# Performance work log

Hardware: AMD Instinct MI355X
Metric: run time of the kernel (lower is better)

## Reference

```python
import jax, jax.numpy as jnp
import numpy as np

N = 1024
H = 1024
B, T = 64, 256


def setup_inputs() -> dict:
    key = jax.random.key(0)
    ks = jax.random.split(key, 12)
    inp = {
        "h_time": jax.random.normal(ks[0], (B, T, H), dtype=jnp.float32),
        "A_pearson": jax.random.uniform(ks[1], (N, N), dtype=jnp.float32),
        "E_dyn": jax.random.normal(ks[2], (N, H), dtype=jnp.float32) * 0.1,
        "alpha_raw": jnp.float32(0.5),
        "tau_raw": jnp.float32(1.0),
        # gate_gen: Linear(H, H//2) -> GELU -> Linear(H//2, N) -> Sigmoid
        "gate_W1": jax.random.normal(ks[3], (H, H // 2), dtype=jnp.float32) * (1.0 / np.sqrt(H)),
        "gate_b1": jnp.zeros((H // 2,), dtype=jnp.float32),
        "gate_W2": jax.random.normal(ks[4], (H // 2, N), dtype=jnp.float32) * (1.0 / np.sqrt(H // 2)),
        "gate_b2": jnp.zeros((N,), dtype=jnp.float32),
        "h2n_W": jax.random.normal(ks[5], (H, N), dtype=jnp.float32) * (1.0 / np.sqrt(H)),
        "h2n_b": jnp.zeros((N,), dtype=jnp.float32),
        "n2h_W": jax.random.normal(ks[6], (N, H), dtype=jnp.float32) * (1.0 / np.sqrt(N)),
        "n2h_b": jnp.zeros((H,), dtype=jnp.float32),
        "ln_w": jnp.ones((H,), dtype=jnp.float32),
        "ln_b": jnp.zeros((H,), dtype=jnp.float32),
    }
    return inp


def _layernorm(x, w, b, eps=1e-5):
    mu = x.mean(-1, keepdims=True)
    var = ((x - mu) ** 2).mean(-1, keepdims=True)
    return (x - mu) * jax.lax.rsqrt(var + eps) * w + b


def reference(h_time, A_pearson, E_dyn, alpha_raw, tau_raw,
              gate_W1, gate_b1, gate_W2, gate_b2,
              h2n_W, h2n_b, n2h_W, n2h_b, ln_w, ln_b):
    tau = jax.nn.softplus(tau_raw) + 1e-6
    alpha = jax.nn.sigmoid(alpha_raw)

    h_mean = h_time.mean(axis=(0, 1))                      # [H]
    E = E_dyn + h_mean[None, :]
    E_cur = E / jnp.maximum(jnp.linalg.norm(E, axis=-1, keepdims=True), 1e-12)  # F.normalize

    A_dyn = jax.nn.relu(E_cur @ E_cur.T)                   # [N,N]
    A_dyn = A_dyn / (A_dyn.sum(axis=-1, keepdims=True) + 1e-6)
    A_dyn = 0.5 * (A_dyn + A_dyn.T)
    A_base = alpha * A_pearson + (1.0 - alpha) * A_dyn

    h_gate = h_time.mean(axis=1)                           # [B,H]
    hid = jax.nn.gelu(h_gate @ gate_W1 + gate_b1, approximate=False)
    gamma = jax.nn.sigmoid(hid @ gate_W2 + gate_b2)        # [B,N]

    # Python loop over batch == row-scaling by mean gate
    A_mix = A_base * gamma.mean(axis=0)[:, None]           # [N,N]

    z_nodes = h_time @ h2n_W + h2n_b                       # [B,T,N]
    z_gcn = jnp.einsum('btn,mn->btm', z_nodes, A_mix)      # z_nodes @ A_mix.T
    msg_h = z_gcn @ n2h_W + n2h_b                          # [B,T,H]

    logits = (A_base @ E_cur) / tau                        # [N,H]
    node_attn = jax.nn.softmax(logits, axis=0)
    global_w = jnp.tanh(node_attn.mean(axis=0))            # [H]

    y = h_time * (1.0 + global_w) + msg_h
    return _layernorm(y, ln_w, ln_b)
```

## Files before the change

kernel.cpp:

```cpp
#include <hip/hip_runtime.h>
#include <math.h>

#define H 1024
#define Nn 1024
#define Bb 64
#define Tt 256
#define BT (Bb * Tt)

typedef unsigned short ushort_t;
typedef __attribute__((ext_vector_type(8))) short bf16x8;
typedef __attribute__((ext_vector_type(4))) float f32x4;


__device__ __forceinline__ ushort_t f2bf(float x) {
    union { float f; unsigned u; } v; v.f = x;
    unsigned r = v.u + 0x7FFFu + ((v.u >> 16) & 1u);
    return (ushort_t)(r >> 16);
}
__device__ __forceinline__ float bf2f(ushort_t h) {
    union { unsigned u; float f; } v; v.u = ((unsigned)h) << 16; return v.f;
}

__device__ __forceinline__ float block_reduce_sum_256(float v) {
    __shared__ float sbuf[4];
    __syncthreads();
    #pragma unroll
    for (int off = 32; off > 0; off >>= 1) v += __shfl_down(v, off, 64);
    int lane = threadIdx.x & 63, w = threadIdx.x >> 6;
    if (lane == 0) sbuf[w] = v;
    __syncthreads();
    if (threadIdx.x == 0) sbuf[0] = sbuf[0] + sbuf[1] + sbuf[2] + sbuf[3];
    __syncthreads();
    return sbuf[0];
}

__global__ void k_stage1(const float* __restrict__ h_time, float* __restrict__ hg_part,
                         ushort_t* __restrict__ ht_bf16, const float* __restrict__ n2h_b,
                         float* __restrict__ rowsumS, float* __restrict__ bias_h,
                         const float* __restrict__ n2h_W, const float* __restrict__ h2n_W,
                         const float* __restrict__ W1, const float* __restrict__ W2,
                         ushort_t* __restrict__ n2hWT_h, ushort_t* __restrict__ n2hWT_l,
                         ushort_t* __restrict__ h2nW_h, ushort_t* __restrict__ h2nW_l,
                         float* __restrict__ W1T, float* __restrict__ W2T) {
    __shared__ float tile[32][33];
    int id = blockIdx.x;
    if (id < 2048) {
        int b = id >> 5, r = id & 31;
        int z = r >> 2, cb = r & 3;
        int col = cb * 256 + threadIdx.x;
        if (b == 0 && z == 0) {
            rowsumS[col] = 0.f;
            bias_h[col] = n2h_b[col];
        }
        float s = 0.f;
        #pragma unroll 4
        for (int t = z * 32; t < z * 32 + 32; ++t) {
            size_t o = ((size_t)b * Tt + t) * H + col;
            float v = h_time[o];
            s += v;
            ht_bf16[o] = f2bf(v);
        }
        hg_part[(size_t)(b * 8 + z) * H + col] = s;
        return;
    }
    int tx = threadIdx.x & 31, ty = threadIdx.x >> 5;
    if (id < 3072) {
        int t = id - 2048;
        int i0 = (t >> 5) * 32, j0 = (t & 31) * 32;
        #pragma unroll
        for (int q = 0; q < 4; ++q)
            tile[ty + 8 * q][tx] = n2h_W[(size_t)(i0 + ty + 8 * q) * H + j0 + tx];
        __syncthreads();
        #pragma unroll
        for (int q = 0; q < 4; ++q) {
            float v = tile[tx][ty + 8 * q];
            size_t o = (size_t)(j0 + ty + 8 * q) * Nn + i0 + tx;
            ushort_t hh = f2bf(v);
            n2hWT_h[o] = hh;
            n2hWT_l[o] = f2bf(v - bf2f(hh));
        }
    } else if (id < 4096) {
        size_t idx = (size_t)(id - 3072) * 1024 + threadIdx.x * 4;
        float4 v = *(const float4*)&h2n_W[idx];
        float c[4] = {v.x, v.y, v.z, v.w};
        union { ushort_t u[4]; uint2 w; } ph, pl;
        #pragma unroll
        for (int q = 0; q < 4; ++q) {
            ph.u[q] = f2bf(c[q]);
            pl.u[q] = f2bf(c[q] - bf2f(ph.u[q]));
        }
        *(uint2*)&h2nW_h[idx] = ph.w;
        *(uint2*)&h2nW_l[idx] = pl.w;
    } else if (id < 4608) {
        int t = id - 4096;
        int i0 = (t >> 4) * 32, j0 = (t & 15) * 32;
        #pragma unroll
        for (int q = 0; q < 4; ++q)
            tile[ty + 8 * q][tx] = W1[(size_t)(i0 + ty + 8 * q) * 512 + j0 + tx];
        __syncthreads();
        #pragma unroll
        for (int q = 0; q < 4; ++q)
            W1T[(size_t)(j0 + ty + 8 * q) * 1024 + i0 + tx] = tile[tx][ty + 8 * q];
    } else {
        int t = id - 4608;
        int i0 = (t >> 5) * 32, j0 = (t & 31) * 32;
        #pragma unroll
        for (int q = 0; q < 4; ++q)
            tile[ty + 8 * q][tx] = W2[(size_t)(i0 + ty + 8 * q) * 1024 + j0 + tx];
        __syncthreads();
        #pragma unroll
        for (int q = 0; q < 4; ++q)
            W2T[(size_t)(j0 + ty + 8 * q) * 512 + i0 + tx] = tile[tx][ty + 8 * q];
    }
}

__global__ void k_stage2(const float* __restrict__ hg_part, float* __restrict__ h_gate,
                         float* __restrict__ h_mean) {
    int id = blockIdx.x;
    if (id < 256) {
        int b = id >> 2, cb = id & 3;
        int col = cb * 256 + threadIdx.x;
        float s = 0.f;
        #pragma unroll
        for (int z = 0; z < 8; ++z) s += hg_part[(size_t)(b * 8 + z) * H + col];
        h_gate[b * H + col] = s * (1.0f / Tt);
    } else {
        int h = (id - 256) * 256 + threadIdx.x;
        float s = 0.f;
        for (int r = 0; r < 512; ++r) s += hg_part[(size_t)r * H + h];
        h_mean[h] = s * (1.0f / (Bb * Tt));
    }
}

__global__ __launch_bounds__(256) void k_stage3(
    const float* __restrict__ E_dyn, const float* __restrict__ h_mean,
    ushort_t* __restrict__ E_b,
    const float* __restrict__ h_gate, const float* __restrict__ W1T,
    const float* __restrict__ b1, float* __restrict__ hid) {
    if (blockIdx.x < 1024) {
        int n = blockIdx.x;
        float e[4]; float ss = 0.f;
        #pragma unroll
        for (int q = 0; q < 4; ++q) {
            int h = threadIdx.x + 256 * q;
            e[q] = E_dyn[(size_t)n * H + h] + h_mean[h];
            ss += e[q] * e[q];
        }
        float tot = block_reduce_sum_256(ss);
        float scale = 1.0f / fmaxf(sqrtf(tot), 1e-12f);
        #pragma unroll
        for (int q = 0; q < 4; ++q) {
            int h = threadIdx.x + 256 * q;
            E_b[(size_t)n * H + h] = f2bf(e[q] * scale);
        }
        return;
    }
    int gid = (blockIdx.x - 1024) * 4 + (threadIdx.x >> 6);
    int lane = threadIdx.x & 63;
    int b = gid >> 9, j = gid & 511;
    const float* xr = h_gate + b * H;
    const float* wr = W1T + (size_t)j * H;
    float s = 0.f;
    #pragma unroll
    for (int it = 0; it < 4; ++it) {
        int k = it * 256 + lane * 4;
        float4 x4 = *(const float4*)&xr[k];
        float4 w4 = *(const float4*)&wr[k];
        s += x4.x * w4.x + x4.y * w4.y + x4.z * w4.z + x4.w * w4.w;
    }
    #pragma unroll
    for (int off = 32; off > 0; off >>= 1) s += __shfl_down(s, off, 64);
    if (lane == 0) {
        float a = s + b1[j];
        hid[b * 512 + j] = 0.5f * a * (1.0f + erff(a * 0.70710678118654752f));
    }
}

template <int PASSES, int EPI>
__device__ __forceinline__ void gemm64_body(
    int bx, int by,
    const ushort_t* __restrict__ Ah, const ushort_t* __restrict__ Al,
    const ushort_t* __restrict__ Bh, const ushort_t* __restrict__ Bl,
    ushort_t* __restrict__ O1, ushort_t* __restrict__ O2,
    float* __restrict__ fout, const float* __restrict__ fvec,
    int M, int N, int K) {
    constexpr int NST = (PASSES == 3) ? 4 : 2;
    constexpr int BUFSZ = NST * 64 * 64;
    __shared__ ushort_t sStage[2 * BUFSZ];
    const int tid = threadIdx.x, wave = tid >> 6, lane = tid & 63;
    const int quad = lane >> 4, l16 = lane & 15;
    const int m0 = by * 64, n0 = bx * 64;
    const int wm = (wave >> 1) * 32, wn = (wave & 1) * 32;
    const int sw = (l16 & 7) << 3;

    f32x4 acc[2][2];
    #pragma unroll
    for (int i = 0; i < 2; ++i)
        #pragma unroll
        for (int j = 0; j < 2; ++j)
            acc[i][j] = (f32x4){0.f, 0.f, 0.f, 0.f};

    auto stage = [&](int buf, int k0) {
        ushort_t* sAh = sStage + buf * BUFSZ;
        ushort_t* sBh = sAh + 64 * 64;
        ushort_t* sAl = sAh + 2 * 64 * 64;
        ushort_t* sBl = sAh + 3 * 64 * 64;
        #pragma unroll
        for (int inst = 0; inst < 2; ++inst) {
            const int cbase = (wave * 2 + inst) * 64;
            const int c = cbase + lane;
            const int row = c >> 3;
            const int q = (c & 7) ^ (row & 7);
            const size_t offA = (size_t)(m0 + row) * K + k0 + q * 8;
            const size_t offB = (size_t)(n0 + row) * K + k0 + q * 8;
            __builtin_amdgcn_global_load_lds(
                (const __attribute__((address_space(1))) unsigned int*)(Ah + offA),
                (__attribute__((address_space(3))) unsigned int*)&sAh[cbase * 8], 16, 0, 0);
            __builtin_amdgcn_global_load_lds(
                (const __attribute__((address_space(1))) unsigned int*)(Bh + offB),
                (__attribute__((address_space(3))) unsigned int*)&sBh[cbase * 8], 16, 0, 0);
            if constexpr (PASSES == 3) {
                __builtin_amdgcn_global_load_lds(
                    (const __attribute__((address_space(1))) unsigned int*)(Al + offA),
                    (__attribute__((address_space(3))) unsigned int*)&sAl[cbase * 8], 16, 0, 0);
                __builtin_amdgcn_global_load_lds(
                    (const __attribute__((address_space(1))) unsigned int*)(Bl + offB),
                    (__attribute__((address_space(3))) unsigned int*)&sBl[cbase * 8], 16, 0, 0);
            }
        }
    };

    auto compute = [&](int buf) {
        const ushort_t* sAh = sStage + buf * BUFSZ;
        const ushort_t* sBh = sAh + 64 * 64;
        const ushort_t* sAl = sAh + 2 * 64 * 64;
        const ushort_t* sBl = sAh + 3 * 64 * 64;
        #pragma unroll
        for (int half = 0; half < 2; ++half) {
            bf16x8 fah[2], fbh[2];
            bf16x8 fal[PASSES == 3 ? 2 : 1], fbl[PASSES == 3 ? 2 : 1];
            #pragma unroll
            for (int i = 0; i < 2; ++i) {
                const int ko = ((half * 4 + quad) << 3) ^ sw;
                fah[i] = *(const bf16x8*)&sAh[(wm + i * 16 + l16) * 64 + ko];
                fbh[i] = *(const bf16x8*)&sBh[(wn + i * 16 + l16) * 64 + ko];
                if constexpr (PASSES == 3) {
                    fal[i] = *(const bf16x8*)&sAl[(wm + i * 16 + l16) * 64 + ko];
                    fbl[i] = *(const bf16x8*)&sBl[(wn + i * 16 + l16) * 64 + ko];
                }
            }
            #pragma unroll
            for (int i = 0; i < 2; ++i)
                #pragma unroll
                for (int j = 0; j < 2; ++j) {
                    acc[i][j] = __builtin_amdgcn_mfma_f32_16x16x32_bf16(fah[i], fbh[j], acc[i][j], 0, 0, 0);
                    if constexpr (PASSES == 3) {
                        acc[i][j] = __builtin_amdgcn_mfma_f32_16x16x32_bf16(fah[i], fbl[j], acc[i][j], 0, 0, 0);
                        acc[i][j] = __builtin_amdgcn_mfma_f32_16x16x32_bf16(fal[i], fbh[j], acc[i][j], 0, 0, 0);
                    }
                }
        }
    };

    stage(0, 0);
    __syncthreads();
    int cur = 0;
    for (int k0 = 64; k0 < K; k0 += 64) {
        stage(cur ^ 1, k0);
        compute(cur);
        __syncthreads();
        cur ^= 1;
    }
    compute(cur);

    float fv[2];
    if constexpr (EPI == 2) {
        #pragma unroll
        for (int j = 0; j < 2; ++j) fv[j] = fvec[n0 + wn + j * 16 + l16];
    }
    #pragma unroll
    for (int i = 0; i < 2; ++i)
        #pragma unroll
        for (int r = 0; r < 4; ++r) {
            const int m = m0 + wm + i * 16 + quad * 4 + r;
            float rowacc = 0.f;
            #pragma unroll
            for (int j = 0; j < 2; ++j) {
                const size_t o = (size_t)m * N + n0 + wn + j * 16 + l16;
                float v = acc[i][j][r];
                if constexpr (EPI == 1) {
                    v = fmaxf(v, 0.f);
                    O1[o] = f2bf(v);
                    rowacc += v;
                } else if constexpr (EPI == 2) {
                    ushort_t hh = f2bf(v);
                    O1[o] = hh;
                    O2[o] = f2bf(v - bf2f(hh));
                    rowacc += v * fv[j];
                } else {
                    O1[o] = f2bf(v);
                }
            }
            if constexpr (EPI == 1 || EPI == 2) {
                rowacc += __shfl_xor(rowacc, 1);
                rowacc += __shfl_xor(rowacc, 2);
                rowacc += __shfl_xor(rowacc, 4);
                rowacc += __shfl_xor(rowacc, 8);
                if (l16 == 0) atomicAdd(&fout[m], rowacc);
            }
        }
}

__global__ __launch_bounds__(256) void k_stage4(
    const float* __restrict__ hid, const float* __restrict__ W2T,
    const float* __restrict__ b2, float* __restrict__ gmean,
    const ushort_t* __restrict__ E_b, ushort_t* __restrict__ Sb,
    float* __restrict__ rowsumS) {
    if (blockIdx.x < 256) {
        int n = blockIdx.x * 4 + (threadIdx.x >> 6);
        int lane = threadIdx.x & 63;
        const float* wr = W2T + (size_t)n * 512;
        float4 w0 = *(const float4*)&wr[lane * 4];
        float4 w1 = *(const float4*)&wr[256 + lane * 4];
        float bb = b2[n];
        float acc = 0.f;
        for (int b = 0; b < Bb; ++b) {
            const float* xr = hid + b * 512;
            float4 x0 = *(const float4*)&xr[lane * 4];
            float4 x1 = *(const float4*)&xr[256 + lane * 4];
            float s = x0.x * w0.x + x0.y * w0.y + x0.z * w0.z + x0.w * w0.w
                    + x1.x * w1.x + x1.y * w1.y + x1.z * w1.z + x1.w * w1.w;
            #pragma unroll
            for (int off = 32; off > 0; off >>= 1) s += __shfl_down(s, off, 64);
            if (lane == 0) acc += 1.0f / (1.0f + expf(-(s + bb)));
        }
        if (lane == 0) gmean[n] = acc * (1.0f / Bb);
        return;
    }
    int t = blockIdx.x - 256;
    gemm64_body<1, 1>(t & 15, t >> 4, E_b, nullptr, E_b, nullptr,
                      Sb, nullptr, rowsumS, nullptr, Nn, Nn, H);
}

__global__ void k_amixT(const ushort_t* __restrict__ Sb, const float* __restrict__ A_p,
                        const float* __restrict__ rowsumS, const float* __restrict__ gmean,
                        const float* __restrict__ alpha_raw,
                        ushort_t* __restrict__ Th, ushort_t* __restrict__ Tl) {
    __shared__ float tile[32][33];
    int i0 = blockIdx.y * 32, j0 = blockIdx.x * 32;
    int tx = threadIdx.x & 31, ty = threadIdx.x >> 5;
    float alpha = 1.0f / (1.0f + expf(-alpha_raw[0]));
    #pragma unroll
    for (int q = 0; q < 4; ++q) {
        int i = i0 + ty + 8 * q, j = j0 + tx;
        size_t idx = (size_t)i * Nn + j;
        float s = bf2f(Sb[idx]);
        float ad = 0.5f * s * (1.0f / (rowsumS[i] + 1e-6f) + 1.0f / (rowsumS[j] + 1e-6f));
        tile[ty + 8 * q][tx] = gmean[i] * fmaf(alpha, A_p[idx], (1.0f - alpha) * ad);
    }
    __syncthreads();
    #pragma unroll
    for (int q = 0; q < 4; ++q) {
        float v = tile[tx][ty + 8 * q];
        size_t o = (size_t)(j0 + ty + 8 * q) * Nn + i0 + tx;
        ushort_t hh = f2bf(v);
        Th[o] = hh;
        Tl[o] = f2bf(v - bf2f(hh));
    }
}

__global__ __launch_bounds__(256) void k_c1t(
    const ushort_t* __restrict__ Ah, const ushort_t* __restrict__ Al,
    const ushort_t* __restrict__ Bh, const ushort_t* __restrict__ Bl,
    ushort_t* __restrict__ O1, ushort_t* __restrict__ O2,
    float* __restrict__ fout, const float* __restrict__ fvec) {
    gemm64_body<3, 2>(blockIdx.x & 15, blockIdx.x >> 4, Ah, Al, Bh, Bl, O1, O2, fout, fvec,
                      Nn, Nn, Nn);
}
__global__ __launch_bounds__(256) void k_c2t(
    const ushort_t* __restrict__ Ah, const ushort_t* __restrict__ Al,
    const ushort_t* __restrict__ Bh, const ushort_t* __restrict__ Bl,
    ushort_t* __restrict__ O1) {
    gemm64_body<3, 3>(blockIdx.x & 15, blockIdx.x >> 4, Ah, Al, Bh, Bl, O1, nullptr,
                      nullptr, nullptr, Nn, Nn, Nn);
}

__global__ __launch_bounds__(256) void gemm_big(
    const ushort_t* __restrict__ A, const ushort_t* __restrict__ Bt,
    float* __restrict__ fout, const float* __restrict__ fvec,
    int M, int N, int K) {
    constexpr int BUFSZ = 2 * 128 * 64;
    __shared__ ushort_t sStage[2 * BUFSZ];

    const int tid = threadIdx.x;
    const int wave = tid >> 6, lane = tid & 63;
    const int quad = lane >> 4, l16 = lane & 15;
    int bx = blockIdx.x, g = bx & 7, s = bx >> 3;
    const int m0 = (g * 16 + (s >> 3)) * 128;
    const int n0 = (s & 7) * 128;
    const int wm = (wave >> 1) * 64, wn = (wave & 1) * 64;
    const int sw = (l16 & 7) << 3;

    f32x4 acc[4][4];
    #pragma unroll
    for (int i = 0; i < 4; ++i)
        #pragma unroll
        for (int j = 0; j < 4; ++j)
            acc[i][j] = (f32x4){0.f, 0.f, 0.f, 0.f};

    auto stage = [&](int buf, int k0) {
        ushort_t* sAh = sStage + buf * BUFSZ;
        ushort_t* sBh = sAh + 128 * 64;
        #pragma unroll
        for (int inst = 0; inst < 4; ++inst) {
            const int cbase = (wave * 4 + inst) * 64;
            const int c = cbase + lane;
            const int row = c >> 3;
            const int q = (c & 7) ^ (row & 7);
            const size_t offA = (size_t)(m0 + row) * K + k0 + q * 8;
            const size_t offB = (size_t)(n0 + row) * K + k0 + q * 8;
            __builtin_amdgcn_global_load_lds(
                (const __attribute__((address_space(1))) unsigned int*)(A + offA),
                (__attribute__((address_space(3))) unsigned int*)&sAh[cbase * 8], 16, 0, 0);
            __builtin_amdgcn_global_load_lds(
                (const __attribute__((address_space(1))) unsigned int*)(Bt + offB),
                (__attribute__((address_space(3))) unsigned int*)&sBh[cbase * 8], 16, 0, 0);
        }
    };

    auto compute = [&](int buf) {
        const ushort_t* sAh = sStage + buf * BUFSZ;
        const ushort_t* sBh = sAh + 128 * 64;
        #pragma unroll
        for (int half = 0; half < 2; ++half) {
            bf16x8 fah[4], fbh[4];
            #pragma unroll
            for (int i = 0; i < 4; ++i) {
                const int ko = ((half * 4 + quad) << 3) ^ sw;
                fah[i] = *(const bf16x8*)&sAh[(wm + i * 16 + l16) * 64 + ko];
                fbh[i] = *(const bf16x8*)&sBh[(wn + i * 16 + l16) * 64 + ko];
            }
            #pragma unroll
            for (int i = 0; i < 4; ++i)
                #pragma unroll
                for (int j = 0; j < 4; ++j)
                    acc[i][j] = __builtin_amdgcn_mfma_f32_16x16x32_bf16(fah[i], fbh[j], acc[i][j], 0, 0, 0);
        }
    };

    stage(0, 0);
    __syncthreads();
    int cur = 0;
    for (int k0 = 64; k0 < K; k0 += 64) {
        stage(cur ^ 1, k0);
        compute(cur);
        __syncthreads();
        cur ^= 1;
    }
    compute(cur);
    __syncthreads();

    float* EsW = (float*)sStage + wave * 4096;
    const float SC = 1.0009765622f;

    #pragma unroll
    for (int i = 0; i < 4; ++i)
        #pragma unroll
        for (int j = 0; j < 4; ++j)
            #pragma unroll
            for (int r = 0; r < 4; ++r)
                EsW[i * 1024 + (quad * 4 + r) * 64 + j * 16 + l16] = acc[i][j][r];
    __syncthreads();
    #pragma unroll
    for (int i = 0; i < 4; ++i) {
        #pragma unroll
        for (int it = 0; it < 4; ++it) {
            const int idx = it * 64 + lane;
            const int row = idx >> 4, f4 = idx & 15;
            const int m = m0 + wm + i * 16 + row;
            const int coln = n0 + wn + f4 * 4;
            float4 v = *(const float4*)&EsW[i * 1024 + row * 64 + f4 * 4];
            float4 b4 = *(const float4*)&fvec[coln];
            ushort4 h4 = *(const ushort4*)&A[(size_t)m * N + coln];
            float4 y;
            y.x = v.x + b4.x + SC * bf2f(h4.x);
            y.y = v.y + b4.y + SC * bf2f(h4.y);
            y.z = v.z + b4.z + SC * bf2f(h4.z);
            y.w = v.w + b4.w + SC * bf2f(h4.w);
            *(float4*)&fout[(size_t)m * N + coln] = y;
        }
    }
}

__global__ __launch_bounds__(256) void k_final_ln(const float* __restrict__ ln_w,
                                                  const float* __restrict__ ln_b,
                                                  float* __restrict__ out) {
    int wave = threadIdx.x >> 6, lane = threadIdx.x & 63;
    size_t row = (size_t)blockIdx.x * 4 + wave;
    float4 v[4];
    float s = 0.f;
    #pragma unroll
    for (int q = 0; q < 4; ++q) {
        v[q] = *(const float4*)&out[row * H + q * 256 + lane * 4];
        s += v[q].x + v[q].y + v[q].z + v[q].w;
    }
    #pragma unroll
    for (int off = 1; off < 64; off <<= 1) s += __shfl_xor(s, off, 64);
    float mu = s * (1.0f / H);
    float ss = 0.f;
    #pragma unroll
    for (int q = 0; q < 4; ++q) {
        v[q].x -= mu; v[q].y -= mu; v[q].z -= mu; v[q].w -= mu;
        ss += v[q].x * v[q].x + v[q].y * v[q].y + v[q].z * v[q].z + v[q].w * v[q].w;
    }
    #pragma unroll
    for (int off = 1; off < 64; off <<= 1) ss += __shfl_xor(ss, off, 64);
    float rstd = rsqrtf(ss * (1.0f / H) + 1e-5f);
    #pragma unroll
    for (int q = 0; q < 4; ++q) {
        int k = q * 256 + lane * 4;
        float4 w4 = *(const float4*)&ln_w[k];
        float4 b4 = *(const float4*)&ln_b[k];
        float4 o;
        o.x = fmaf(v[q].x * rstd, w4.x, b4.x);
        o.y = fmaf(v[q].y * rstd, w4.y, b4.y);
        o.z = fmaf(v[q].z * rstd, w4.z, b4.z);
        o.w = fmaf(v[q].w * rstd, w4.w, b4.w);
        *(float4*)&out[row * H + k] = o;
    }
}


extern "C" void kernel_launch(void* const* d_in, const int* in_sizes, int n_in,
                              void* d_out, int out_size, void* d_ws, size_t ws_size,
                              hipStream_t stream) {
    const float* h_time    = (const float*)d_in[0];
    const float* A_p       = (const float*)d_in[1];
    const float* E_dyn     = (const float*)d_in[2];
    const float* alpha_raw = (const float*)d_in[3];
    const float* gW1   = (const float*)d_in[5];
    const float* gb1   = (const float*)d_in[6];
    const float* gW2   = (const float*)d_in[7];
    const float* gb2   = (const float*)d_in[8];
    const float* h2n_W = (const float*)d_in[9];
    const float* h2n_b = (const float*)d_in[10];
    const float* n2h_W = (const float*)d_in[11];
    const float* n2h_b = (const float*)d_in[12];
    const float* ln_w  = (const float*)d_in[13];
    const float* ln_b  = (const float*)d_in[14];
    float* out = (float*)d_out;

    float* ws = (float*)d_ws;
    float* h_gate  = ws;  ws += Bb * H;
    float* h_mean  = ws;  ws += H;
    float* rowsumS = ws;  ws += Nn;
    float* bias_h  = ws;  ws += H;
    float* hid     = ws;  ws += Bb * 512;
    float* gmean   = ws;  ws += Nn;
    float* W1T     = ws;  ws += 512 * H;
    float* W2T     = ws;  ws += H * 512;
    float* hg_part = ws;  ws += 512 * H;
    ws += 256;
    ushort_t* E_b     = (ushort_t*)ws;  ws += (Nn * H) / 2;
    ushort_t* Sb      = (ushort_t*)ws;  ws += (Nn * Nn) / 2;
    ushort_t* AmixT_h = (ushort_t*)ws;  ws += (Nn * Nn) / 2;
    ushort_t* AmixT_l = (ushort_t*)ws;  ws += (Nn * Nn) / 2;
    ushort_t* n2hWT_h = (ushort_t*)ws;  ws += (Nn * H) / 2;
    ushort_t* n2hWT_l = (ushort_t*)ws;  ws += (Nn * H) / 2;
    ushort_t* h2nW_h  = (ushort_t*)ws;  ws += (H * Nn) / 2;
    ushort_t* h2nW_l  = (ushort_t*)ws;  ws += (H * Nn) / 2;
    ushort_t* C1Th    = (ushort_t*)ws;  ws += (H * Nn) / 2;
    ushort_t* C1Tl    = (ushort_t*)ws;  ws += (H * Nn) / 2;
    ushort_t* C2t     = (ushort_t*)ws;  ws += (H * H) / 2;
    ushort_t* ht      = (ushort_t*)ws;  ws += ((size_t)BT * H) / 2;

    k_stage1<<<5120, 256, 0, stream>>>(h_time, hg_part, ht, n2h_b, rowsumS, bias_h,
                                       n2h_W, h2n_W, gW1, gW2,
                                       n2hWT_h, n2hWT_l, h2nW_h, h2nW_l, W1T, W2T);
    k_stage2<<<260, 256, 0, stream>>>(hg_part, h_gate, h_mean);
    k_stage3<<<9216, 256, 0, stream>>>(E_dyn, h_mean, E_b, h_gate, W1T, gb1, hid);
    k_stage4<<<512, 256, 0, stream>>>(hid, W2T, gb2, gmean, E_b, Sb, rowsumS);
    k_amixT<<<dim3(32, 32), 256, 0, stream>>>(Sb, A_p, rowsumS, gmean, alpha_raw, AmixT_h, AmixT_l);
    k_c1t<<<256, 256, 0, stream>>>(n2hWT_h, n2hWT_l, AmixT_h, AmixT_l, C1Th, C1Tl, bias_h, h2n_b);
    k_c2t<<<256, 256, 0, stream>>>(C1Th, C1Tl, h2nW_h, h2nW_l, C2t);
    gemm_big<<<1024, 256, 0, stream>>>(ht, C2t, out, bias_h, BT, H, H);
    k_final_ln<<<4096, 256, 0, stream>>>(ln_w, ln_b, out);
}
```

Baseline: 316.6 us.

## Enlarge big GEMM tiles to 256x256 with 8 waves and barrier-synchronized MFMA phases

The main BTxHxH bf16 GEMM moves from 128x128 tiles with 4 waves to 256x256 tiles with 8 waves, so each wave computes a 128x64 sub-tile. The k-loop is restructured with explicit s_barrier, waitcnt and setprio around MFMA bursts so waves interleave LDS reads and matrix math. The epilogue is split into two passes to fit the larger tile in LDS. The aim is to raise arithmetic intensity and cut global/L2 traffic per FLOP. The cost is only 256 blocks (about one wave of work on the GPU), higher register pressure, and a dropped grouped-tile swizzle for L2 locality.

```diff
diff --git a/kernel.cpp b/kernel.cpp
--- a/kernel.cpp
+++ b/kernel.cpp
@@ -385,110 +385,126 @@
                       nullptr, nullptr, Nn, Nn, Nn);
 }
 
-__global__ __launch_bounds__(256) void gemm_big(
+__global__ __launch_bounds__(512, 2) void gemm_big(
     const ushort_t* __restrict__ A, const ushort_t* __restrict__ Bt,
     float* __restrict__ fout, const float* __restrict__ fvec,
     int M, int N, int K) {
-    constexpr int BUFSZ = 2 * 128 * 64;
+    constexpr int BUFSZ = 2 * 256 * 64;
     __shared__ ushort_t sStage[2 * BUFSZ];
 
     const int tid = threadIdx.x;
     const int wave = tid >> 6, lane = tid & 63;
     const int quad = lane >> 4, l16 = lane & 15;
-    int bx = blockIdx.x, g = bx & 7, s = bx >> 3;
-    const int m0 = (g * 16 + (s >> 3)) * 128;
-    const int n0 = (s & 7) * 128;
-    const int wm = (wave >> 1) * 64, wn = (wave & 1) * 64;
-    const int sw = (l16 & 7) << 3;
-
-    f32x4 acc[4][4];
-    #pragma unroll
-    for (int i = 0; i < 4; ++i)
+    const int wr = wave >> 2, wc = wave & 3;
+    const int m0 = (blockIdx.x >> 2) * 256;
+    const int n0 = (blockIdx.x & 3) * 256;
+    const int wm = wr * 128, wn = wc * 64;
+    const int swz = l16 & 7;
+
+    f32x4 acc[8][4];
+    #pragma unroll
+    for (int i = 0; i < 8; ++i)
         #pragma unroll
         for (int j = 0; j < 4; ++j)
             acc[i][j] = (f32x4){0.f, 0.f, 0.f, 0.f};
 
     auto stage = [&](int buf, int k0) {
-        ushort_t* sAh = sStage + buf * BUFSZ;
-        ushort_t* sBh = sAh + 128 * 64;
-        #pragma unroll
-        for (int inst = 0; inst < 4; ++inst) {
-            const int cbase = (wave * 4 + inst) * 64;
-            const int c = cbase + lane;
+        ushort_t* sA = sStage + buf * BUFSZ;
+        ushort_t* sB = sA + 256 * 64;
+        #pragma unroll
+        for (int pass = 0; pass < 4; ++pass) {
+            const int c = pass * 512 + tid;
             const int row = c >> 3;
             const int q = (c & 7) ^ (row & 7);
             const size_t offA = (size_t)(m0 + row) * K + k0 + q * 8;
             const size_t offB = (size_t)(n0 + row) * K + k0 + q * 8;
             __builtin_amdgcn_global_load_lds(
                 (const __attribute__((address_space(1))) unsigned int*)(A + offA),
-                (__attribute__((address_space(3))) unsigned int*)&sAh[cbase * 8], 16, 0, 0);
+                (__attribute__((address_space(3))) unsigned int*)&sA[c * 8], 16, 0, 0);
             __builtin_amdgcn_global_load_lds(
                 (const __attribute__((address_space(1))) unsigned int*)(Bt + offB),
-                (__attribute__((address_space(3))) unsigned int*)&sBh[cbase * 8], 16, 0, 0);
+                (__attribute__((address_space(3))) unsigned int*)&sB[c * 8], 16, 0, 0);
         }
     };
 
-    auto compute = [&](int buf) {
-        const ushort_t* sAh = sStage + buf * BUFSZ;
-        const ushort_t* sBh = sAh + 128 * 64;
-        #pragma unroll
-        for (int half = 0; half < 2; ++half) {
-            bf16x8 fah[4], fbh[4];
-            #pragma unroll
-            for (int i = 0; i < 4; ++i) {
-                const int ko = ((half * 4 + quad) << 3) ^ sw;
-                fah[i] = *(const bf16x8*)&sAh[(wm + i * 16 + l16) * 64 + ko];
-                fbh[i] = *(const bf16x8*)&sBh[(wn + i * 16 + l16) * 64 + ko];
+    stage(0, 0);
+    int buf = 0;
+    for (int t = 0; t < 16; ++t) {
+        __syncthreads();
+        if (t + 1 < 16) stage(buf ^ 1, (t + 1) * 64);
+        const ushort_t* sA = sStage + buf * BUFSZ;
+        const ushort_t* sB = sA + 256 * 64;
+        #pragma unroll
+        for (int s = 0; s < 2; ++s) {
+            bf16x8 fb[4];
+            #pragma unroll
+            for (int j = 0; j < 4; ++j) {
+                const int row = wn + j * 16 + l16;
+                const int ch = (s * 4 + quad) ^ swz;
+                fb[j] = *(const bf16x8*)&sB[row * 64 + ch * 8];
             }
             #pragma unroll
-            for (int i = 0; i < 4; ++i)
+            for (int mh = 0; mh < 2; ++mh) {
+                bf16x8 fa[4];
                 #pragma unroll
-                for (int j = 0; j < 4; ++j)
-                    acc[i][j] = __builtin_amdgcn_mfma_f32_16x16x32_bf16(fah[i], fbh[j], acc[i][j], 0, 0, 0);
-        }
-    };
-
-    stage(0, 0);
+                for (int i = 0; i < 4; ++i) {
+                    const int row = wm + mh * 64 + i * 16 + l16;
+                    const int ch = (s * 4 + quad) ^ swz;
+                    fa[i] = *(const bf16x8*)&sA[row * 64 + ch * 8];
+                }
+                __builtin_amdgcn_s_barrier();
+                asm volatile("s_waitcnt lgkmcnt(0)" ::: "memory");
+                __builtin_amdgcn_sched_barrier(0);
+                __builtin_amdgcn_s_setprio(1);
+                #pragma unroll
+                for (int i = 0; i < 4; ++i)
+                    #pragma unroll
+                    for (int j = 0; j < 4; ++j)
+                        acc[mh * 4 + i][j] =
+                            __builtin_amdgcn_mfma_f32_16x16x32_bf16(fa[i], fb[j], acc[mh * 4 + i][j], 0, 0, 0);
+                __builtin_amdgcn_s_setprio(0);
+                __builtin_amdgcn_s_barrier();
+            }
+        }
+        buf ^= 1;
+    }
     __syncthreads();
-    int cur = 0;
-    for (int k0 = 64; k0 < K; k0 += 64) {
-        stage(cur ^ 1, k0);
-        compute(cur);
+
+    float* Es = (float*)sStage + wave * 4096;
+    const float SC = 1.0009765622f;
+
+    #pragma unroll
+    for (int pass = 0; pass < 2; ++pass) {
+        #pragma unroll
+        for (int ii = 0; ii < 4; ++ii) {
+            const int i = pass * 4 + ii;
+            #pragma unroll
+            for (int j = 0; j < 4; ++j)
+                #pragma unroll
+                for (int r = 0; r < 4; ++r)
+                    Es[ii * 1024 + (quad * 4 + r) * 64 + j * 16 + l16] = acc[i][j][r];
+        }
         __syncthreads();
-        cur ^= 1;
-    }
-    compute(cur);
-    __syncthreads();
-
-    float* EsW = (float*)sStage + wave * 4096;
-    const float SC = 1.0009765622f;
-
-    #pragma unroll
-    for (int i = 0; i < 4; ++i)
-        #pragma unroll
-        for (int j = 0; j < 4; ++j)
-            #pragma unroll
-            for (int r = 0; r < 4; ++r)
-                EsW[i * 1024 + (quad * 4 + r) * 64 + j * 16 + l16] = acc[i][j][r];
-    __syncthreads();
-    #pragma unroll
-    for (int i = 0; i < 4; ++i) {
-        #pragma unroll
-        for (int it = 0; it < 4; ++it) {
-            const int idx = it * 64 + lane;
-            const int row = idx >> 4, f4 = idx & 15;
-            const int m = m0 + wm + i * 16 + row;
-            const int coln = n0 + wn + f4 * 4;
-            float4 v = *(const float4*)&EsW[i * 1024 + row * 64 + f4 * 4];
-            float4 b4 = *(const float4*)&fvec[coln];
-            ushort4 h4 = *(const ushort4*)&A[(size_t)m * N + coln];
-            float4 y;
-            y.x = v.x + b4.x + SC * bf2f(h4.x);
-            y.y = v.y + b4.y + SC * bf2f(h4.y);
-            y.z = v.z + b4.z + SC * bf2f(h4.z);
-            y.w = v.w + b4.w + SC * bf2f(h4.w);
-            *(float4*)&fout[(size_t)m * N + coln] = y;
-        }
+        #pragma unroll
+        for (int ii = 0; ii < 4; ++ii) {
+            #pragma unroll
+            for (int it = 0; it < 4; ++it) {
+                const int idx = it * 64 + lane;
+                const int row = idx >> 4, f4 = idx & 15;
+                const int m = m0 + wm + (pass * 4 + ii) * 16 + row;
+                const int coln = n0 + wn + f4 * 4;
+                float4 v = *(const float4*)&Es[ii * 1024 + row * 64 + f4 * 4];
+                float4 b4 = *(const float4*)&fvec[coln];
+                ushort4 h4 = *(const ushort4*)&A[(size_t)m * N + coln];
+                float4 y;
+                y.x = v.x + b4.x + SC * bf2f(h4.x);
+                y.y = v.y + b4.y + SC * bf2f(h4.y);
+                y.z = v.z + b4.z + SC * bf2f(h4.z);
+                y.w = v.w + b4.w + SC * bf2f(h4.w);
+                *(float4*)&fout[(size_t)m * N + coln] = y;
+            }
+        }
+        __syncthreads();
     }
 }
 
@@ -583,6 +599,6 @@
     k_amixT<<<dim3(32, 32), 256, 0, stream>>>(Sb, A_p, rowsumS, gmean, alpha_raw, AmixT_h, AmixT_l);
     k_c1t<<<256, 256, 0, stream>>>(n2hWT_h, n2hWT_l, AmixT_h, AmixT_l, C1Th, C1Tl, bias_h, h2n_b);
     k_c2t<<<256, 256, 0, stream>>>(C1Th, C1Tl, h2nW_h, h2nW_l, C2t);
-    gemm_big<<<1024, 256, 0, stream>>>(ht, C2t, out, bias_h, BT, H, H);
+    gemm_big<<<256, 512, 0, stream>>>(ht, C2t, out, bias_h, BT, H, H);
     k_final_ln<<<4096, 256, 0, stream>>>(ln_w, ln_b, out);
 }
```

After: 318.8 us. No clear change (+0.7%).
